# Performance work log

Measured on AMD Instinct MI355X. Metric: run time of the kernel, lower is better.

Reference implementation:

```python
import jax, jax.numpy as jnp
import numpy as np

B, IN_C, OUT_C, H, W = 16, 64, 64, 128, 128
MIN_R, MAX_R, BASE, SCALE = 1, 6, 3, 3


def setup_inputs() -> dict:
    key = jax.random.key(0)
    k1, k2 = jax.random.split(key)
    x = jax.random.normal(k1, (B, IN_C, H, W), dtype=jnp.float32)
    # kaiming-uniform-ish scale for a 3x3 conv weight
    weight = jax.random.normal(k2, (OUT_C, IN_C, 3, 3), dtype=jnp.float32) * (1.0 / np.sqrt(IN_C * 9))
    # truncated-normal-style integer dilation per output channel (deterministic)
    rng = np.random.default_rng(0)
    offsets = np.clip(np.round(rng.normal(BASE, SCALE, size=OUT_C)), MIN_R, MAX_R).astype(np.int32)
    return {"x": x, "weight": weight, "offsets": offsets}


def _gsd_conv(x, weight, offs_np):
    # Per-channel dilation conv: group channels by dilation, conv each group
    # (dilation=o, padding=o keeps HxW), scatter back to original channel order.
    out = jnp.zeros((x.shape[0], weight.shape[0], x.shape[2], x.shape[3]), dtype=x.dtype)
    for o in np.unique(offs_np):
        idx = np.nonzero(offs_np == o)[0]          # static channel indices for this dilation
        w = weight[idx]                             # [g, in_c, 3, 3]
        o = int(o)
        y = jax.lax.conv_general_dilated(
            x, w,
            window_strides=(1, 1),
            padding=[(o, o), (o, o)],
            rhs_dilation=(o, o),
            dimension_numbers=("NCHW", "OIHW", "NCHW"),
        )                                           # [B, g, H, W]
        out = out.at[:, idx].set(y)
    return out


def reference(x, weight, offsets):
    offs_np = np.asarray(offsets)
    return _gsd_conv(x, weight, offs_np)
```

## Files before the change

### kernel.cpp

```cpp
#include <hip/hip_runtime.h>


#define HW_ 128
#define C_ 64
#define B_ 16
#define EX 44
#define EY 28
#define NPIX (EY * EX)
#define CHPP (NPIX * 2)
#define NSETS 39
#define PLANEDW (NSETS * 64 * 4)
#define HDW (NPIX * 4)
#define PADW 140
#define PLANE_STRIDE (PADW * PADW * 16)
#define MAX_ITEMS 12
#define WS_WPACK_OFF 1024
#define WS_XB16_OFF (1 << 20)
#define XB16_BYTES ((size_t)B_ * 4 * PLANE_STRIDE * 2)


typedef __attribute__((ext_vector_type(8))) short short8;
typedef __attribute__((ext_vector_type(16))) float floatx16;

__device__ __forceinline__ unsigned bf16rne(float f) {
  unsigned u = __float_as_uint(f);
  return (u + 0x7FFFu + ((u >> 16) & 1u)) >> 16;
}

#define GLOAD_LDS16(g, l)                                   \
  __builtin_amdgcn_global_load_lds(                         \
      (const __attribute__((address_space(1))) void*)(g),   \
      (__attribute__((address_space(3))) void*)(l), 16, 0, 0)

__global__ __launch_bounds__(256) void gsd_prep(
    const float* __restrict__ x, const int* __restrict__ offsets,
    const float* __restrict__ w, int* __restrict__ desc,
    uint4* __restrict__ wpack, unsigned short* __restrict__ xb16,
    const int nrow) {
  const int bid = blockIdx.x;
  const int tid = threadIdx.x;

  if (bid < nrow) {
    const int b = bid / PADW, py = bid - b * PADW;
    uint4* o4 = (uint4*)xb16;
    const size_t pb0 = ((size_t)b * 4) * 39200 + (size_t)py * 280;
    const uint4 z = make_uint4(0, 0, 0, 0);
    if (py < 6 || py >= PADW - 6) {
      for (int i = tid; i < 1120; i += 256) {
        const int ks = i / 280, r = i - ks * 280;
        o4[pb0 + (size_t)ks * 39200 + r] = z;
      }
      return;
    }
    if (tid < 96) {
      const int ks = tid / 24, rr = tid - ks * 24;
      const int idx = rr < 12 ? rr : 256 + rr;
      o4[pb0 + (size_t)ks * 39200 + idx] = z;
    }
    const int y = py - 6;
    __shared__ unsigned l32[128 * 33];
    const int xx = tid & 127, ph = tid >> 7;
    const float* xp = x + (size_t)b * (C_ * HW_ * HW_) + y * HW_ + xx;
#pragma unroll 4
    for (int p = ph; p < 32; p += 2) {
      const float v0 = xp[(2 * p) * (HW_ * HW_)];
      const float v1 = xp[(2 * p + 1) * (HW_ * HW_)];
      l32[xx * 33 + p] = bf16rne(v0) | (bf16rne(v1) << 16);
    }
    __syncthreads();
#pragma unroll 4
    for (int ch = tid; ch < 1024; ch += 256) {
      const int ks = ch >> 8, r = ch & 255;
      const unsigned* s = &l32[(r >> 1) * 33 + ks * 8 + (r & 1) * 4];
      o4[pb0 + (size_t)ks * 39200 + 12 + r] = make_uint4(s[0], s[1], s[2], s[3]);
    }
    return;
  }

  __shared__ int sd[128];
  __shared__ int soffs[C_];
  if (tid < C_) soffs[tid] = offsets[tid];
  __syncthreads();
  if (tid < C_) {
    const int key = soffs[tid];
    int rank = 0;
    for (int c = 0; c < C_; ++c) {
      const int kc = soffs[c];
      rank += (int)((kc < key) | ((kc == key) & (c < tid)));
    }
    sd[rank] = tid;
  }
  __syncthreads();
  if (tid == 0) {
    int ni = 0;
    for (int t = 0; t < 2; ++t) {
      int cnt = 0, prev = -1;
      for (int m = 0; m < 32; ++m) {
        const int dd = soffs[sd[t * 32 + m]];
        if (dd != prev && cnt < 6 && ni < MAX_ITEMS) {
          sd[66 + t * 6 + cnt] = dd;
          sd[78 + t * 6 + cnt] = ni;
          sd[91 + ni * 2] = t;
          sd[92 + ni * 2] = dd;
          ++ni;
          ++cnt;
          prev = dd;
        }
      }
      sd[64 + t] = cnt;
    }
    sd[90] = ni;
  }
  __syncthreads();

  const int sbid = bid - nrow;
  if (sbid == 0) {
    if (tid < 91) desc[tid] = sd[tid];
    return;
  }
  const int wix = sbid - 1;
  if (wix >= sd[90]) return;
  const int o = sd[91 + wix * 2];
  const int dit = sd[92 + wix * 2];

  for (int i = tid; i < 4 * 9 * 64; i += 256) {
    const int ks = i / 576;
    const int r = i % 576;
    const int tap = r >> 6;
    const int lane = r & 63;
    const int m = lane & 31, hh = lane >> 5;
    const int oc = sd[o * 32 + m];
    const bool act = (soffs[oc] == dit);
    unsigned ww[4];
    for (int jj = 0; jj < 4; ++jj) {
      float v0 = 0.f, v1 = 0.f;
      if (act) {
        const int ic0 = ks * 16 + hh * 8 + jj * 2;
        v0 = w[(oc * C_ + ic0) * 9 + tap];
        v1 = w[(oc * C_ + ic0 + 1) * 9 + tap];
      }
      ww[jj] = bf16rne(v0) | (bf16rne(v1) << 16);
    }
    wpack[(size_t)wix * 2304 + i] = make_uint4(ww[0], ww[1], ww[2], ww[3]);
  }
}

template <bool PRE>
__global__ __launch_bounds__(512, 4) void gsd_conv(
    const float* __restrict__ x, const unsigned short* __restrict__ xb16,
    const int* __restrict__ desc, const uint4* __restrict__ wpack,
    float* __restrict__ out) {
  const int tid = threadIdx.x;
  const int bid0 = blockIdx.x;
  const int gxid = (bid0 & 7) * 64 + (bid0 >> 3);
  const int b = gxid >> 5;
  const int yt = (gxid >> 2) & 7;
  const int xt = gxid & 3;
  const int y0 = yt * 16, x0 = xt * 32;

  const int lane = tid & 63;
  const int n = lane & 31;
  const int h = lane >> 5;
  const int wv = tid >> 6;
  const int o = wv >> 2;
  const int rq = wv & 3;

  __shared__ __align__(16) unsigned ldsbuf[2][PLANEDW];

  floatx16 acc[4];
#pragma unroll
  for (int rt = 0; rt < 4; ++rt)
#pragma unroll
    for (int e = 0; e < 16; ++e) acc[rt][e] = 0.f;

  const unsigned short* xbase;
  int srcoff[5];
  if constexpr (PRE) {
    xbase = xb16 + (size_t)b * 4 * PLANE_STRIDE;
#pragma unroll
    for (int j = 0; j < 5; ++j) {
      int q = (wv + j * 8) * 64 + lane;
      if (q > CHPP - 1) q = CHPP - 1;
      const int p = q >= NPIX ? 1 : 0;
      const int pix = q - p * NPIX;
      const int yy = pix / EX, xx = pix - yy * EX;
      srcoff[j] = ((y0 + yy) * PADW + (x0 + xx)) * 16 + p * 8;
    }
  }
  int slx, sq, sy2, gxc;
  bool xin;
  const float* xb;
  if constexpr (!PRE) {
    slx = tid & 63;
    sq = (tid >> 6) & 3;
    sy2 = tid >> 8;
    xb = x + (size_t)b * (C_ * HW_ * HW_);
    const int gx = x0 - 6 + slx;
    gxc = gx < 0 ? 0 : (gx > 127 ? 127 : gx);
    xin = ((unsigned)gx < 128u) & (slx < EX);
  }

  const int cnt = __builtin_amdgcn_readfirstlane(desc[64 + o]);

  auto STAGE = [&](int buf, int ks) {
    if constexpr (PRE) {
      const unsigned short* xp = xbase + (size_t)ks * PLANE_STRIDE;
#pragma unroll
      for (int j = 0; j < 5; ++j) {
        if (j < 4 || wv < 7) {
          GLOAD_LDS16(xp + srcoff[j], &ldsbuf[buf][(wv + j * 8) * 256]);
        }
      }
    }
  };

  auto COMPUTE = [&](const unsigned* cbuf, int ks) {
    const unsigned* cb = cbuf + h * HDW;
    for (int s = 0; s < cnt; ++s) {
      const int d = __builtin_amdgcn_readfirstlane(desc[66 + o * 6 + s]);
      const int wix = __builtin_amdgcn_readfirstlane(desc[78 + o * 6 + s]);
      const uint4* wp = wpack + ((size_t)wix * 4 + ks) * 576 + lane;
#pragma unroll
      for (int tap = 0; tap < 9; ++tap) {
        const int ky = tap / 3 - 1, kx = tap % 3 - 1;
        const short8 af = __builtin_bit_cast(short8, wp[tap * 64]);
        const int prowb = rq * 4 + ky * d + 6;
        const int pxb = n + kx * d + 6;
#pragma unroll
        for (int rt = 0; rt < 4; ++rt) {
          const int pix = (prowb + rt) * EX + pxb;
          const short8 bf = *reinterpret_cast<const short8*>(&cb[pix * 4]);
          acc[rt] = __builtin_amdgcn_mfma_f32_32x32x16_bf16(af, bf, acc[rt],
                                                            0, 0, 0);
        }
      }
    }
  };

  if constexpr (PRE) {
    STAGE(0, 0);
    __syncthreads();
#pragma unroll
    for (int ks = 0; ks < 3; ++ks) {
      STAGE((ks + 1) & 1, ks + 1);
      COMPUTE(ldsbuf[ks & 1], ks);
      __syncthreads();
    }
    COMPUTE(ldsbuf[1], 3);
  } else {
    for (int ks = 0; ks < 4; ++ks) {
      if (ks) __syncthreads();
      const float* xp = xb + (size_t)(ks * 16 + sq * 4) * (HW_ * HW_);
#pragma unroll 2
      for (int yy = sy2; yy < EY; yy += 2) {
        const int gy = y0 - 6 + yy;
        const int gyc = gy < 0 ? 0 : (gy > 127 ? 127 : gy);
        const bool ok = xin & ((unsigned)gy < 128u);
        const float* p = xp + gyc * HW_ + gxc;
        float v0 = p[0];
        float v1 = p[HW_ * HW_];
        float v2 = p[2 * HW_ * HW_];
        float v3 = p[3 * HW_ * HW_];
        if (!ok) { v0 = v1 = v2 = v3 = 0.f; }
        const unsigned lo = bf16rne(v0) | (bf16rne(v1) << 16);
        const unsigned hi = bf16rne(v2) | (bf16rne(v3) << 16);
        if (slx < EX) {
          const int pix = yy * EX + slx;
          const int dws = (sq >> 1) * HDW + pix * 4 + ((sq & 1) << 1);
          *reinterpret_cast<uint2*>(&ldsbuf[0][dws]) = make_uint2(lo, hi);
        }
      }
      __syncthreads();
      COMPUTE(ldsbuf[0], ks);
    }
  }

  int oc[16];
#pragma unroll
  for (int reg = 0; reg < 16; ++reg) {
    const int row = (reg & 3) + 8 * (reg >> 2) + 4 * h;
    oc[reg] = desc[o * 32 + row];
  }
#pragma unroll
  for (int rt = 0; rt < 4; ++rt) {
    const int y = y0 + rq * 4 + rt;
#pragma unroll
    for (int reg = 0; reg < 16; ++reg) {
      out[((size_t)(b * C_ + oc[reg]) * HW_ + y) * HW_ + x0 + n] =
          acc[rt][reg];
    }
  }
}

extern "C" void kernel_launch(void* const* d_in, const int* in_sizes, int n_in,
                              void* d_out, int out_size, void* d_ws,
                              size_t ws_size, hipStream_t stream) {
  const float* x = (const float*)d_in[0];
  const float* w = (const float*)d_in[1];
  const int* offsets = (const int*)d_in[2];
  float* out = (float*)d_out;

  int* desc = (int*)d_ws;
  uint4* wpack = (uint4*)((char*)d_ws + WS_WPACK_OFF);
  unsigned short* xb16 = (unsigned short*)((char*)d_ws + WS_XB16_OFF);

  const bool pre = ws_size >= (size_t)WS_XB16_OFF + XB16_BYTES;
  const int nrow = pre ? B_ * PADW : 0;

  gsd_prep<<<dim3(nrow + 1 + MAX_ITEMS), 256, 0, stream>>>(
      x, offsets, w, desc, wpack, xb16, nrow);
  if (pre) {
    gsd_conv<true><<<dim3(B_ * 8 * 4), 512, 0, stream>>>(
        x, xb16, desc, wpack, out);
  } else {
    gsd_conv<false><<<dim3(B_ * 8 * 4), 512, 0, stream>>>(
        x, xb16, desc, wpack, out);
  }
}
```

Measured before the change: 182.6 us.

## Double conv block to 1024 threads with two row tiles per wave

Each block now has 16 waves instead of 8, and each wave accumulates two output rows instead of four. Each wave gets half the work and far fewer accumulator registers, which is meant to add latency hiding and cut register pressure. Per segment, the nine weight fragments are now loaded into registers before the MFMA loop. In exchange, each weight fragment is reused across only two MFMAs rather than four, so total weight traffic per output doubles. The launch bound of (1024, 4) asks for more resident waves than the hardware or the LDS budget can hold, which may make the compiler tighten the register limit.

```diff
diff --git a/kernel.cpp b/kernel.cpp
--- a/kernel.cpp
+++ b/kernel.cpp
@@ -146,7 +146,7 @@
 }
 
 template <bool PRE>
-__global__ __launch_bounds__(512, 4) void gsd_conv(
+__global__ __launch_bounds__(1024, 4) void gsd_conv(
     const float* __restrict__ x, const unsigned short* __restrict__ xb16,
     const int* __restrict__ desc, const uint4* __restrict__ wpack,
     float* __restrict__ out) {
@@ -162,24 +162,23 @@
   const int n = lane & 31;
   const int h = lane >> 5;
   const int wv = tid >> 6;
-  const int o = wv >> 2;
-  const int rq = wv & 3;
+  const int o = wv >> 3;
+  const int yp = wv & 7;
+  const int yb = yp * 2;
 
   __shared__ __align__(16) unsigned ldsbuf[2][PLANEDW];
 
-  floatx16 acc[4];
-#pragma unroll
-  for (int rt = 0; rt < 4; ++rt)
-#pragma unroll
-    for (int e = 0; e < 16; ++e) acc[rt][e] = 0.f;
+  floatx16 acc0, acc1;
+#pragma unroll
+  for (int e = 0; e < 16; ++e) { acc0[e] = 0.f; acc1[e] = 0.f; }
 
   const unsigned short* xbase;
-  int srcoff[5];
+  int srcoff[3];
   if constexpr (PRE) {
     xbase = xb16 + (size_t)b * 4 * PLANE_STRIDE;
 #pragma unroll
-    for (int j = 0; j < 5; ++j) {
-      int q = (wv + j * 8) * 64 + lane;
+    for (int j = 0; j < 3; ++j) {
+      int q = (wv + j * 16) * 64 + lane;
       if (q > CHPP - 1) q = CHPP - 1;
       const int p = q >= NPIX ? 1 : 0;
       const int pix = q - p * NPIX;
@@ -187,13 +186,14 @@
       srcoff[j] = ((y0 + yy) * PADW + (x0 + xx)) * 16 + p * 8;
     }
   }
-  int slx, sq, sy2, gxc;
+  int slx, sq, sy4, gxc;
   bool xin;
   const float* xb;
   if constexpr (!PRE) {
     slx = tid & 63;
-    sq = (tid >> 6) & 3;
-    sy2 = tid >> 8;
+    const int grp = tid >> 6;
+    sq = grp & 3;
+    sy4 = grp >> 2;
     xb = x + (size_t)b * (C_ * HW_ * HW_);
     const int gx = x0 - 6 + slx;
     gxc = gx < 0 ? 0 : (gx > 127 ? 127 : gx);
@@ -206,9 +206,9 @@
     if constexpr (PRE) {
       const unsigned short* xp = xbase + (size_t)ks * PLANE_STRIDE;
 #pragma unroll
-      for (int j = 0; j < 5; ++j) {
-        if (j < 4 || wv < 7) {
-          GLOAD_LDS16(xp + srcoff[j], &ldsbuf[buf][(wv + j * 8) * 256]);
+      for (int j = 0; j < 3; ++j) {
+        if (j < 2 || wv < 7) {
+          GLOAD_LDS16(xp + srcoff[j], &ldsbuf[buf][(wv + j * 16) * 256]);
         }
       }
     }
@@ -220,19 +220,21 @@
       const int d = __builtin_amdgcn_readfirstlane(desc[66 + o * 6 + s]);
       const int wix = __builtin_amdgcn_readfirstlane(desc[78 + o * 6 + s]);
       const uint4* wp = wpack + ((size_t)wix * 4 + ks) * 576 + lane;
+      uint4 af[9];
+#pragma unroll
+      for (int t = 0; t < 9; ++t) af[t] = wp[t * 64];
 #pragma unroll
       for (int tap = 0; tap < 9; ++tap) {
         const int ky = tap / 3 - 1, kx = tap % 3 - 1;
-        const short8 af = __builtin_bit_cast(short8, wp[tap * 64]);
-        const int prowb = rq * 4 + ky * d + 6;
+        const short8 a8 = __builtin_bit_cast(short8, af[tap]);
+        const int prow = yb + ky * d + 6;
         const int pxb = n + kx * d + 6;
-#pragma unroll
-        for (int rt = 0; rt < 4; ++rt) {
-          const int pix = (prowb + rt) * EX + pxb;
-          const short8 bf = *reinterpret_cast<const short8*>(&cb[pix * 4]);
-          acc[rt] = __builtin_amdgcn_mfma_f32_32x32x16_bf16(af, bf, acc[rt],
-                                                            0, 0, 0);
-        }
+        const int pix0 = prow * EX + pxb;
+        const short8 bf0 = *reinterpret_cast<const short8*>(&cb[pix0 * 4]);
+        const short8 bf1 =
+            *reinterpret_cast<const short8*>(&cb[(pix0 + EX) * 4]);
+        acc0 = __builtin_amdgcn_mfma_f32_32x32x16_bf16(a8, bf0, acc0, 0, 0, 0);
+        acc1 = __builtin_amdgcn_mfma_f32_32x32x16_bf16(a8, bf1, acc1, 0, 0, 0);
       }
     }
   };
@@ -251,8 +253,7 @@
     for (int ks = 0; ks < 4; ++ks) {
       if (ks) __syncthreads();
       const float* xp = xb + (size_t)(ks * 16 + sq * 4) * (HW_ * HW_);
-#pragma unroll 2
-      for (int yy = sy2; yy < EY; yy += 2) {
+      for (int yy = sy4; yy < EY; yy += 4) {
         const int gy = y0 - 6 + yy;
         const int gyc = gy < 0 ? 0 : (gy > 127 ? 127 : gy);
         const bool ok = xin & ((unsigned)gy < 128u);
@@ -275,20 +276,13 @@
     }
   }
 
-  int oc[16];
 #pragma unroll
   for (int reg = 0; reg < 16; ++reg) {
     const int row = (reg & 3) + 8 * (reg >> 2) + 4 * h;
-    oc[reg] = desc[o * 32 + row];
-  }
-#pragma unroll
-  for (int rt = 0; rt < 4; ++rt) {
-    const int y = y0 + rq * 4 + rt;
-#pragma unroll
-    for (int reg = 0; reg < 16; ++reg) {
-      out[((size_t)(b * C_ + oc[reg]) * HW_ + y) * HW_ + x0 + n] =
-          acc[rt][reg];
-    }
+    const int oc = desc[o * 32 + row];
+    float* op = &out[((size_t)(b * C_ + oc) * HW_ + (y0 + yb)) * HW_ + x0 + n];
+    op[0] = acc0[reg];
+    op[HW_] = acc1[reg];
   }
 }
 
@@ -310,10 +304,10 @@
   gsd_prep<<<dim3(nrow + 1 + MAX_ITEMS), 256, 0, stream>>>(
       x, offsets, w, desc, wpack, xb16, nrow);
   if (pre) {
-    gsd_conv<true><<<dim3(B_ * 8 * 4), 512, 0, stream>>>(
+    gsd_conv<true><<<dim3(B_ * 8 * 4), 1024, 0, stream>>>(
         x, xb16, desc, wpack, out);
   } else {
-    gsd_conv<false><<<dim3(B_ * 8 * 4), 512, 0, stream>>>(
+    gsd_conv<false><<<dim3(B_ * 8 * 4), 1024, 0, stream>>>(
         x, xb16, desc, wpack, out);
   }
 }
```

New measurement: 187.3 us. 2.6% more time.
